# Optimization experiments

Measured on AMD Instinct MI355X. Metric: run time of the kernel, lower is better.

Reference implementation:

```python
import jax, jax.numpy as jnp
import numpy as np
import math

N_HEAD = 8
D_MODEL = 512
HEAD_SIZE = D_MODEL // N_HEAD
VOCAB = 16384
BLOCK = 512
LN_EPS = 1e-5


def sinusoidal_pe(max_len, dim):
    pos = np.arange(max_len)[:, None].astype(np.float32)
    div = np.exp(np.arange(0, dim, 2).astype(np.float32) * (-math.log(10000.0) / dim))
    pe = np.zeros((max_len, dim), dtype=np.float32)
    pe[:, 0::2] = np.sin(pos * div)
    pe[:, 1::2] = np.cos(pos * div)
    return jnp.asarray(pe)  # (max_len, hs)


def setup_inputs() -> dict:
    key = jax.random.key(0)
    ks = jax.random.split(key, 6)
    b, t = 4, BLOCK
    return {
        "x": jax.random.normal(ks[0], (b, t, 1), dtype=jnp.float32),
        "embedding": jax.random.normal(ks[1], (N_HEAD, VOCAB, HEAD_SIZE), dtype=jnp.float32),
        "enc_w": jax.random.normal(ks[2], (D_MODEL, 1), dtype=jnp.float32) * 0.05,
        "enc_b": jax.random.normal(ks[3], (D_MODEL,), dtype=jnp.float32) * 0.05,
        "ln_w": jnp.ones((HEAD_SIZE,), dtype=jnp.float32),
        "ln_b": jnp.zeros((HEAD_SIZE,), dtype=jnp.float32),
        "dec_w": jax.random.normal(ks[4], (1, D_MODEL), dtype=jnp.float32) * 0.05,
        "dec_b": jax.random.normal(ks[5], (1,), dtype=jnp.float32) * 0.05,
    }


def reference(x, embedding, enc_w, enc_b, ln_w, ln_b, dec_w, dec_b):
    b, t, _ = x.shape
    # encoder: Linear(input_dim -> d_model)
    h = x @ enc_w.T + enc_b                              # (b, t, d_model)
    h = h.reshape(b, t, N_HEAD, HEAD_SIZE).transpose(0, 2, 1, 3)  # (b, nh, t, hs)
    # sinusoidal positional encoding over time, added to head dim
    h = h + sinusoidal_pe(BLOCK, HEAD_SIZE)[:t]
    # LayerNorm over hs
    mu = h.mean(-1, keepdims=True)
    var = ((h - mu) ** 2).mean(-1, keepdims=True)
    h = (h - mu) * jax.lax.rsqrt(var + LN_EPS) * ln_w + ln_b
    # attention over shared per-head codebook
    scores = jnp.einsum('bnth,nvh->bntv', h, embedding) / math.sqrt(D_MODEL)
    probs = jax.nn.softmax(scores, axis=-1)              # (b, nh, t, vocab)
    quant = jnp.einsum('bntv,nvh->bnth', probs, embedding)
    quant = quant.transpose(0, 2, 1, 3).reshape(b, t, D_MODEL)
    # decoder: Linear(d_model -> output_dim)
    return quant @ dec_w.T + dec_b                       # (b, t, 1)
```

## Files before the change

kernel.cpp:

```cpp
#include <hip/hip_runtime.h>
#include <hip/hip_bf16.h>
#include <math.h>

#define NH 8
#define HS 64
#define VOCAB 16384
#define QPH 2048
#define NSLICE 32
#define QSCALE (0.04419417382415922f * 1.4426950408889634f)

typedef __attribute__((ext_vector_type(8))) short bf16x8;
typedef __attribute__((ext_vector_type(4))) float f32x4;

static __device__ __forceinline__ unsigned short f2bf(float f) {
    __hip_bfloat16 h = __float2bfloat16(f);
    unsigned short u;
    __builtin_memcpy(&u, &h, 2);
    return u;
}

static __device__ __forceinline__ float fexp2(float x) {
#if __has_builtin(__builtin_amdgcn_exp2f)
    return __builtin_amdgcn_exp2f(x);
#else
    return __expf(x * 0.6931471805599453f);
#endif
}

static __device__ __forceinline__ void stage16(const void* g, void* l) {
    __builtin_amdgcn_global_load_lds(
        (const __attribute__((address_space(1))) void*)g,
        (__attribute__((address_space(3))) void*)l, 16, 0, 0);
}

__global__ void eprep(const float* __restrict__ emb, const float* __restrict__ dec_w,
                      unsigned short* __restrict__ ebf, float* __restrict__ g) {
    __shared__ float red[256];
    int tid = threadIdx.x;
    int nt  = blockIdx.x;
    int h   = (tid >> 7) & 1;
    int q   = (tid >> 5) & 3;
    int r   = (tid >> 1) & 15;
    int jh  = tid & 1;
    int n   = nt >> 10;
    int T   = nt & 1023;
    int row = n * VOCAB + T * 16 + r;
    int c4  = h * 8 + q * 2 + jh;
    f32x4 vv = ((const f32x4*)emb)[(size_t)row * 16 + c4];
    ushort4 u = make_ushort4(f2bf(vv.x), f2bf(vv.y), f2bf(vv.z), f2bf(vv.w));
    ((ushort4*)ebf)[(size_t)nt * 256 + tid] = u;
    const float* dw = dec_w + n * 64 + c4 * 4;
    float p = vv.x * dw[0] + vv.y * dw[1] + vv.z * dw[2] + vv.w * dw[3];
    red[tid] = p;
    __syncthreads();
    if (tid < 16) {
        float s = 0.f;
        #pragma unroll
        for (int m = 0; m < 16; ++m)
            s += red[((m >> 3) * 128) + (((m & 7) >> 1) * 32) + tid * 2 + (m & 1)];
        g[n * VOCAB + T * 16 + tid] = s;
    }
}

__global__ void qprep(const float* __restrict__ x, const float* __restrict__ enc_w,
                      const float* __restrict__ enc_b, const float* __restrict__ ln_w,
                      const float* __restrict__ ln_b, unsigned short* __restrict__ qbf) {
    int row  = blockIdx.x * 4 + (threadIdx.x >> 6);
    int h    = threadIdx.x & 63;
    int n = row >> 11;
    int q = row & 2047;
    int t = q & 511;
    float xv = x[q];
    int d = n * 64 + h;
    float h2  = (float)(h & ~1);
    float div = __expf(h2 * (-9.210340371976184f / 64.0f));
    float ang = (float)t * div;
    float pe  = (h & 1) ? __cosf(ang) : __sinf(ang);
    float v = xv * enc_w[d] + enc_b[d] + pe;
    float s = v;
    #pragma unroll
    for (int off = 1; off < 64; off <<= 1) s += __shfl_xor(s, off);
    float mu = s * (1.0f / 64.0f);
    float dd = v - mu;
    float s2 = dd * dd;
    #pragma unroll
    for (int off = 1; off < 64; off <<= 1) s2 += __shfl_xor(s2, off);
    float var = s2 * (1.0f / 64.0f);
    float y = dd * rsqrtf(var + 1e-5f) * ln_w[h] + ln_b[h];
    int qt   = (q >> 4) & 7;
    int l15  = q & 15;
    int kf   = h >> 5;
    int quad = (h >> 3) & 3;
    int j    = h & 7;
    size_t idx = ((size_t)(n * 16 + (q >> 7)) * 8192)
               + ((size_t)((qt * 2 + kf) * 4 + quad) * 128) + l15 * 8 + j;
    qbf[idx] = f2bf(y * QSCALE);
}

__global__ void __launch_bounds__(256, 4)
attn(const unsigned short* __restrict__ qbf, const unsigned short* __restrict__ ebf,
     const float* __restrict__ g, float2* __restrict__ part) {
    __shared__ __attribute__((aligned(16))) char smem[16384 + 8192];
    float* gl = (float*)(smem + 16384);

    int tid  = threadIdx.x;
    int w    = tid >> 6;
    int lane = tid & 63;
    int quad = lane >> 4;
    int l15  = lane & 15;
    int head   = blockIdx.x & 7;
    int qgroup = (blockIdx.x >> 3) & 15;
    int vgroup = blockIdx.x >> 7;
    int vslice = vgroup * 4 + w;

    const char*  qsrc = (const char*)qbf + (size_t)(head * 16 + qgroup) * 16384;
    const char*  esrc = (const char*)ebf + (size_t)head * 2097152 + (size_t)vslice * 65536;
    const float* gp   = g + head * VOCAB + vgroup * 2048;

    #pragma unroll
    for (int k = 0; k < 4; ++k)
        stage16(qsrc + k * 4096 + tid * 16, smem + k * 4096 + w * 1024);
    stage16((const char*)gp + tid * 16,        (char*)gl + w * 1024);
    stage16((const char*)gp + 4096 + tid * 16, (char*)gl + 4096 + w * 1024);
    __syncthreads();

    float num[8] = {0.f, 0.f, 0.f, 0.f, 0.f, 0.f, 0.f, 0.f};
    float den[8] = {0.f, 0.f, 0.f, 0.f, 0.f, 0.f, 0.f, 0.f};
    const f32x4 z = {0.f, 0.f, 0.f, 0.f};
    const float* gw = gl + w * 512;

    #pragma clang loop unroll(disable)
    for (int it = 0; it < 8; ++it) {
        asm volatile("" ::: "memory");
        const char* eb = esrc + it * 8192;
        bf16x8 a[4][2];
        #pragma unroll
        for (int vt = 0; vt < 4; ++vt) {
            a[vt][0] = *(const bf16x8*)(eb + vt * 2048 +        lane * 16);
            a[vt][1] = *(const bf16x8*)(eb + vt * 2048 + 1024 + lane * 16);
        }
        f32x4 gv[4];
        #pragma unroll
        for (int vt = 0; vt < 4; ++vt)
            gv[vt] = *(const f32x4*)(gw + it * 64 + vt * 16 + quad * 4);

        #pragma unroll
        for (int qt = 0; qt < 8; ++qt) {
            const char* qb = smem + qt * 2048 + lane * 16;
            bf16x8 q0 = *(const bf16x8*)(qb);
            bf16x8 q1 = *(const bf16x8*)(qb + 1024);
            #pragma unroll
            for (int vt = 0; vt < 4; ++vt) {
                f32x4 acc = __builtin_amdgcn_mfma_f32_16x16x32_bf16(a[vt][0], q0, z, 0, 0, 0);
                acc       = __builtin_amdgcn_mfma_f32_16x16x32_bf16(a[vt][1], q1, acc, 0, 0, 0);
                #pragma unroll
                for (int r = 0; r < 4; ++r) {
                    float p = fexp2(acc[r]);
                    den[qt] += p;
                    num[qt] += p * gv[vt][r];
                }
            }
        }
    }

    #pragma unroll
    for (int qt = 0; qt < 8; ++qt) {
        num[qt] += __shfl_xor(num[qt], 16); num[qt] += __shfl_xor(num[qt], 32);
        den[qt] += __shfl_xor(den[qt], 16); den[qt] += __shfl_xor(den[qt], 32);
    }
    #pragma unroll
    for (int j = 0; j < 2; ++j) {
        int qt = quad * 2 + j;
        int qg = qgroup * 128 + qt * 16 + l15;
        part[((size_t)vslice * NH + head) * QPH + qg] = make_float2(num[qt], den[qt]);
    }
}

__global__ void fin(const float2* __restrict__ part, const float* __restrict__ dec_b,
                    float* __restrict__ out) {
    __shared__ float red[8][32];
    int t  = threadIdx.x;
    int ql = t & 31;
    int n  = t >> 5;
    int q  = blockIdx.x * 32 + ql;
    float nv = 0.f, dv = 0.f;
    #pragma unroll 8
    for (int sl = 0; sl < NSLICE; ++sl) {
        float2 nd = part[((size_t)sl * NH + n) * QPH + q];
        nv += nd.x; dv += nd.y;
    }
    red[n][ql] = nv / dv;
    __syncthreads();
    if (t < 32) {
        float s = dec_b[0];
        #pragma unroll
        for (int m = 0; m < NH; ++m) s += red[m][t];
        out[q] = s;
    }
}

extern "C" void kernel_launch(void* const* d_in, const int* in_sizes, int n_in,
                              void* d_out, int out_size, void* d_ws, size_t ws_size,
                              hipStream_t stream) {
    const float* x     = (const float*)d_in[0];
    const float* emb   = (const float*)d_in[1];
    const float* enc_w = (const float*)d_in[2];
    const float* enc_b = (const float*)d_in[3];
    const float* ln_w  = (const float*)d_in[4];
    const float* ln_b  = (const float*)d_in[5];
    const float* dec_w = (const float*)d_in[6];
    const float* dec_b = (const float*)d_in[7];
    float* out = (float*)d_out;

    char* ws = (char*)d_ws;
    unsigned short* qbf  = (unsigned short*)(ws);
    unsigned short* ebf  = (unsigned short*)(ws + 2097152);
    float*          g    = (float*)(ws + 2097152 + 16777216);
    float2*         part = (float2*)(ws + 2097152 + 16777216 + 524288);

    hipLaunchKernelGGL(eprep, dim3(8192), dim3(256), 0, stream, emb, dec_w, ebf, g);
    hipLaunchKernelGGL(qprep, dim3(4096), dim3(256), 0, stream, x, enc_w, enc_b, ln_w, ln_b, qbf);
    hipLaunchKernelGGL(attn,  dim3(1024), dim3(256), 0, stream, qbf, ebf, g, part);
    hipLaunchKernelGGL(fin,   dim3(64),   dim3(256), 0, stream, part, dec_b, out);
}
```

Before: 141.1 us.

## Halve attention query tile, raise occupancy, coalesce eprep reads and restructure qprep

The attention kernel now processes 64 queries per block instead of 128 and launches twice as many blocks. LDS use is halved, launch bounds are raised to 8 blocks per CU, and the key fragments are loaded per vt tile rather than all held at once, which lowers register pressure. eprep now reads the embedding in a fully coalesced pattern, permutes it through LDS and reduces the dec_w dot product with wave shuffles. qprep computes positional encodings once per time step and loops over heads and batches, writing a new 64-query fragment layout; the cost is that each E fragment is read twice as often across blocks.

```diff
diff --git a/kernel.cpp b/kernel.cpp
--- a/kernel.cpp
+++ b/kernel.cpp
@@ -35,73 +35,71 @@
 
 __global__ void eprep(const float* __restrict__ emb, const float* __restrict__ dec_w,
                       unsigned short* __restrict__ ebf, float* __restrict__ g) {
-    __shared__ float red[256];
+    __shared__ ushort4 lu[256];
+    __shared__ float red[16];
     int tid = threadIdx.x;
     int nt  = blockIdx.x;
-    int h   = (tid >> 7) & 1;
-    int q   = (tid >> 5) & 3;
-    int r   = (tid >> 1) & 15;
-    int jh  = tid & 1;
     int n   = nt >> 10;
-    int T   = nt & 1023;
-    int row = n * VOCAB + T * 16 + r;
-    int c4  = h * 8 + q * 2 + jh;
-    f32x4 vv = ((const f32x4*)emb)[(size_t)row * 16 + c4];
+    int r   = tid >> 4;
+    int c4  = tid & 15;
+    f32x4 vv = ((const f32x4*)emb)[(size_t)nt * 256 + tid];
     ushort4 u = make_ushort4(f2bf(vv.x), f2bf(vv.y), f2bf(vv.z), f2bf(vv.w));
-    ((ushort4*)ebf)[(size_t)nt * 256 + tid] = u;
+    int h = c4 >> 3, q = (c4 >> 1) & 3, jh = c4 & 1;
+    lu[h * 128 + q * 32 + r * 2 + jh] = u;
     const float* dw = dec_w + n * 64 + c4 * 4;
     float p = vv.x * dw[0] + vv.y * dw[1] + vv.z * dw[2] + vv.w * dw[3];
-    red[tid] = p;
+    p += __shfl_xor(p, 1); p += __shfl_xor(p, 2);
+    p += __shfl_xor(p, 4); p += __shfl_xor(p, 8);
+    if (c4 == 0) red[r] = p;
     __syncthreads();
-    if (tid < 16) {
-        float s = 0.f;
-        #pragma unroll
-        for (int m = 0; m < 16; ++m)
-            s += red[((m >> 3) * 128) + (((m & 7) >> 1) * 32) + tid * 2 + (m & 1)];
-        g[n * VOCAB + T * 16 + tid] = s;
-    }
+    ((ushort4*)ebf)[(size_t)nt * 256 + tid] = lu[tid];
+    if (tid < 16) g[n * VOCAB + (nt & 1023) * 16 + tid] = red[tid];
 }
 
 __global__ void qprep(const float* __restrict__ x, const float* __restrict__ enc_w,
                       const float* __restrict__ enc_b, const float* __restrict__ ln_w,
                       const float* __restrict__ ln_b, unsigned short* __restrict__ qbf) {
-    int row  = blockIdx.x * 4 + (threadIdx.x >> 6);
-    int h    = threadIdx.x & 63;
-    int n = row >> 11;
-    int q = row & 2047;
-    int t = q & 511;
-    float xv = x[q];
-    int d = n * 64 + h;
+    int w = threadIdx.x >> 6;
+    int h = threadIdx.x & 63;
+    int t = blockIdx.x * 4 + w;
     float h2  = (float)(h & ~1);
     float div = __expf(h2 * (-9.210340371976184f / 64.0f));
     float ang = (float)t * div;
     float pe  = (h & 1) ? __cosf(ang) : __sinf(ang);
-    float v = xv * enc_w[d] + enc_b[d] + pe;
-    float s = v;
+    float lw = ln_w[h], lb = ln_b[h];
+    int kf = h >> 5, quad = (h >> 3) & 3, j = h & 7;
+    int fragoff = ((kf * 4 + quad) * 128) + j;
     #pragma unroll
-    for (int off = 1; off < 64; off <<= 1) s += __shfl_xor(s, off);
-    float mu = s * (1.0f / 64.0f);
-    float dd = v - mu;
-    float s2 = dd * dd;
-    #pragma unroll
-    for (int off = 1; off < 64; off <<= 1) s2 += __shfl_xor(s2, off);
-    float var = s2 * (1.0f / 64.0f);
-    float y = dd * rsqrtf(var + 1e-5f) * ln_w[h] + ln_b[h];
-    int qt   = (q >> 4) & 7;
-    int l15  = q & 15;
-    int kf   = h >> 5;
-    int quad = (h >> 3) & 3;
-    int j    = h & 7;
-    size_t idx = ((size_t)(n * 16 + (q >> 7)) * 8192)
-               + ((size_t)((qt * 2 + kf) * 4 + quad) * 128) + l15 * 8 + j;
-    qbf[idx] = f2bf(y * QSCALE);
-}
-
-__global__ void __launch_bounds__(256, 4)
+    for (int n = 0; n < NH; ++n) {
+        float ew = enc_w[n * 64 + h];
+        float eb = enc_b[n * 64 + h];
+        #pragma unroll
+        for (int b = 0; b < 4; ++b) {
+            int q = b * 512 + t;
+            float v = x[q] * ew + eb + pe;
+            float s = v;
+            #pragma unroll
+            for (int off = 1; off < 64; off <<= 1) s += __shfl_xor(s, off);
+            float mu = s * (1.0f / 64.0f);
+            float dd = v - mu;
+            float s2 = dd * dd;
+            #pragma unroll
+            for (int off = 1; off < 64; off <<= 1) s2 += __shfl_xor(s2, off);
+            float var = s2 * (1.0f / 64.0f);
+            float y = dd * rsqrtf(var + 1e-5f) * lw + lb;
+            int qt = (q >> 4) & 3, l15 = q & 15;
+            size_t idx = ((size_t)(n * 32 + (q >> 6)) * 4096)
+                       + qt * 1024 + l15 * 8 + fragoff;
+            qbf[idx] = f2bf(y * QSCALE);
+        }
+    }
+}
+
+__global__ void __launch_bounds__(256, 8)
 attn(const unsigned short* __restrict__ qbf, const unsigned short* __restrict__ ebf,
      const float* __restrict__ g, float2* __restrict__ part) {
-    __shared__ __attribute__((aligned(16))) char smem[16384 + 8192];
-    float* gl = (float*)(smem + 16384);
+    __shared__ __attribute__((aligned(16))) char smem[8192 + 8192];
+    float* gl = (float*)(smem + 8192);
 
     int tid  = threadIdx.x;
     int w    = tid >> 6;
@@ -109,71 +107,58 @@
     int quad = lane >> 4;
     int l15  = lane & 15;
     int head   = blockIdx.x & 7;
-    int qgroup = (blockIdx.x >> 3) & 15;
-    int vgroup = blockIdx.x >> 7;
+    int qgroup = (blockIdx.x >> 3) & 31;
+    int vgroup = blockIdx.x >> 8;
     int vslice = vgroup * 4 + w;
 
-    const char*  qsrc = (const char*)qbf + (size_t)(head * 16 + qgroup) * 16384;
+    const char*  qsrc = (const char*)qbf + (size_t)(head * 32 + qgroup) * 8192;
     const char*  esrc = (const char*)ebf + (size_t)head * 2097152 + (size_t)vslice * 65536;
     const float* gp   = g + head * VOCAB + vgroup * 2048;
 
-    #pragma unroll
-    for (int k = 0; k < 4; ++k)
-        stage16(qsrc + k * 4096 + tid * 16, smem + k * 4096 + w * 1024);
+    stage16(qsrc + tid * 16,        smem + w * 1024);
+    stage16(qsrc + 4096 + tid * 16, smem + 4096 + w * 1024);
     stage16((const char*)gp + tid * 16,        (char*)gl + w * 1024);
     stage16((const char*)gp + 4096 + tid * 16, (char*)gl + 4096 + w * 1024);
     __syncthreads();
 
-    float num[8] = {0.f, 0.f, 0.f, 0.f, 0.f, 0.f, 0.f, 0.f};
-    float den[8] = {0.f, 0.f, 0.f, 0.f, 0.f, 0.f, 0.f, 0.f};
+    float num[4] = {0.f, 0.f, 0.f, 0.f};
+    float den[4] = {0.f, 0.f, 0.f, 0.f};
     const f32x4 z = {0.f, 0.f, 0.f, 0.f};
     const float* gw = gl + w * 512;
 
     #pragma clang loop unroll(disable)
     for (int it = 0; it < 8; ++it) {
-        asm volatile("" ::: "memory");
         const char* eb = esrc + it * 8192;
-        bf16x8 a[4][2];
         #pragma unroll
         for (int vt = 0; vt < 4; ++vt) {
-            a[vt][0] = *(const bf16x8*)(eb + vt * 2048 +        lane * 16);
-            a[vt][1] = *(const bf16x8*)(eb + vt * 2048 + 1024 + lane * 16);
-        }
-        f32x4 gv[4];
-        #pragma unroll
-        for (int vt = 0; vt < 4; ++vt)
-            gv[vt] = *(const f32x4*)(gw + it * 64 + vt * 16 + quad * 4);
-
-        #pragma unroll
-        for (int qt = 0; qt < 8; ++qt) {
-            const char* qb = smem + qt * 2048 + lane * 16;
-            bf16x8 q0 = *(const bf16x8*)(qb);
-            bf16x8 q1 = *(const bf16x8*)(qb + 1024);
+            asm volatile("" ::: "memory");
+            bf16x8 a0 = *(const bf16x8*)(eb + vt * 2048 +        lane * 16);
+            bf16x8 a1 = *(const bf16x8*)(eb + vt * 2048 + 1024 + lane * 16);
+            f32x4 gv  = *(const f32x4*)(gw + it * 64 + vt * 16 + quad * 4);
             #pragma unroll
-            for (int vt = 0; vt < 4; ++vt) {
-                f32x4 acc = __builtin_amdgcn_mfma_f32_16x16x32_bf16(a[vt][0], q0, z, 0, 0, 0);
-                acc       = __builtin_amdgcn_mfma_f32_16x16x32_bf16(a[vt][1], q1, acc, 0, 0, 0);
+            for (int qt = 0; qt < 4; ++qt) {
+                const char* qb = smem + qt * 2048 + lane * 16;
+                bf16x8 q0 = *(const bf16x8*)(qb);
+                bf16x8 q1 = *(const bf16x8*)(qb + 1024);
+                f32x4 acc = __builtin_amdgcn_mfma_f32_16x16x32_bf16(a0, q0, z, 0, 0, 0);
+                acc       = __builtin_amdgcn_mfma_f32_16x16x32_bf16(a1, q1, acc, 0, 0, 0);
                 #pragma unroll
                 for (int r = 0; r < 4; ++r) {
                     float p = fexp2(acc[r]);
                     den[qt] += p;
-                    num[qt] += p * gv[vt][r];
+                    num[qt] += p * gv[r];
                 }
             }
         }
     }
 
     #pragma unroll
-    for (int qt = 0; qt < 8; ++qt) {
+    for (int qt = 0; qt < 4; ++qt) {
         num[qt] += __shfl_xor(num[qt], 16); num[qt] += __shfl_xor(num[qt], 32);
         den[qt] += __shfl_xor(den[qt], 16); den[qt] += __shfl_xor(den[qt], 32);
     }
-    #pragma unroll
-    for (int j = 0; j < 2; ++j) {
-        int qt = quad * 2 + j;
-        int qg = qgroup * 128 + qt * 16 + l15;
-        part[((size_t)vslice * NH + head) * QPH + qg] = make_float2(num[qt], den[qt]);
-    }
+    int qg = qgroup * 64 + quad * 16 + l15;
+    part[((size_t)vslice * NH + head) * QPH + qg] = make_float2(num[quad], den[quad]);
 }
 
 __global__ void fin(const float2* __restrict__ part, const float* __restrict__ dec_b,
@@ -184,7 +169,7 @@
     int n  = t >> 5;
     int q  = blockIdx.x * 32 + ql;
     float nv = 0.f, dv = 0.f;
-    #pragma unroll 8
+    #pragma unroll
     for (int sl = 0; sl < NSLICE; ++sl) {
         float2 nd = part[((size_t)sl * NH + n) * QPH + q];
         nv += nd.x; dv += nd.y;
@@ -219,7 +204,7 @@
     float2*         part = (float2*)(ws + 2097152 + 16777216 + 524288);
 
     hipLaunchKernelGGL(eprep, dim3(8192), dim3(256), 0, stream, emb, dec_w, ebf, g);
-    hipLaunchKernelGGL(qprep, dim3(4096), dim3(256), 0, stream, x, enc_w, enc_b, ln_w, ln_b, qbf);
-    hipLaunchKernelGGL(attn,  dim3(1024), dim3(256), 0, stream, qbf, ebf, g, part);
+    hipLaunchKernelGGL(qprep, dim3(128),  dim3(256), 0, stream, x, enc_w, enc_b, ln_w, ln_b, qbf);
+    hipLaunchKernelGGL(attn,  dim3(2048), dim3(256), 0, stream, qbf, ebf, g, part);
     hipLaunchKernelGGL(fin,   dim3(64),   dim3(256), 0, stream, part, dec_b, out);
 }
```

New measurement: 157.5 us. +11.6%, slower.
